# Kernel tuning notes

Measured on AMD Instinct MI355X. Metric: run time of the kernel, lower is better.

Reference implementation:

```python
import jax, jax.numpy as jnp
import numpy as np

N = 20000; E = 320000; G = 64; C_IN = 128; H = 128; L = 3; S = 4
EPS = 1e-5; SLOPE = 0.01  # GraphNorm eps, leaky_relu negative slope


def _kruskal(ei, ew, n):
    # Kruskal MST over edges sorted by usage-count weight; returns bidirectional MST edges
    # and the updated usage counts (used edges get +1), mirroring kruskal_mst_track_usage.
    order = np.argsort(ew, kind='stable')
    s = ei[0][order]; d = ei[1][order]
    parent = np.arange(n)
    def find(u):
        while parent[u] != u:
            parent[u] = parent[parent[u]]
            u = parent[u]
        return u
    mst = []; used = []
    for i in range(s.shape[0]):
        ru = find(s[i]); rv = find(d[i])
        if ru != rv:
            parent[ru] = rv
            mst.append((s[i], d[i]))
            used.append(order[i])
            if len(mst) == n - 1:
                break
    ew = ew.copy(); ew[np.asarray(used)] += 1
    m = np.asarray(mst, dtype=np.int64).T  # [2, ~n-1]
    return np.concatenate([m, m[::-1]], axis=1), ew  # bidirectional


def setup_inputs():
    rng = np.random.default_rng(0)
    x = rng.standard_normal((N, C_IN), dtype=np.float32)
    edge_index = rng.integers(0, N, size=(2, E)).astype(np.int64)
    batch = np.sort(rng.integers(0, G, size=N)).astype(np.int64)
    # split_graph: shuffle edges, then repeatedly extract MSTs (no_grad / CPU in original)
    perm = rng.permutation(E)
    ei_p = edge_index[:, perm]
    ew = np.zeros(E, dtype=np.int64)
    msts = []
    for _ in range(S - 1):  # only splits 0..3 are used; split 0 is the shuffled full graph
        m, ew = _kruskal(ei_p, ew, N)
        msts.append(m)
    def gp(shape):
        return jnp.asarray((0.05 * rng.standard_normal(shape)).astype(np.float32))
    return {
        'x': jnp.asarray(x),
        'emb_W': gp((C_IN, H)), 'emb_b': gp((H,)),
        'main_W': gp((L, H, H)), 'main_b': gp((L, H)),
        'main_gw': jnp.ones((L, H), jnp.float32), 'main_gb': jnp.zeros((L, H), jnp.float32), 'main_gms': jnp.ones((L, H), jnp.float32),
        'loc_W': gp((L, H, H)), 'loc_b': gp((L, H)),
        'loc_gw': jnp.ones((L, H), jnp.float32), 'loc_gb': jnp.zeros((L, H), jnp.float32), 'loc_gms': jnp.ones((L, H), jnp.float32),
        'merge_W': gp((H * (S + 1), H)), 'merge_b': gp((H,)),
        'edge_index': jnp.asarray(edge_index),
        'edges0': jnp.asarray(ei_p),
        'edges1': jnp.asarray(msts[0]),
        'edges2': jnp.asarray(msts[1]),
        'edges3': jnp.asarray(msts[2]),
        'batch': jnp.asarray(batch),
    }


def _seg(v, idx, n):
    return jax.ops.segment_sum(v, idx, num_segments=n)


def _gcn(x, W, b, src, dst):
    # PyG GCNConv with self-loops and symmetric normalization
    n = x.shape[0]
    h = x @ W
    deg = _seg(jnp.ones(src.shape[0], x.dtype), dst, n) + 1.0
    dinv = jax.lax.rsqrt(deg)
    coef = (dinv[src] * dinv[dst])[:, None]
    out = _seg(h[src] * coef, dst, n) + h * (dinv * dinv)[:, None]  # neighbors + self-loop
    return out + b


def _graph_norm(x, batch, cnt, w, b, ms):
    # PyG GraphNorm: per-graph mean with learnable mean_scale, per-graph variance
    mean = _seg(x, batch, G) / cnt
    out = x - ms * mean[batch]
    var = _seg(out * out, batch, G) / cnt
    inv = jax.lax.rsqrt(var + EPS)
    return w * out * inv[batch] + b


def _gnn(x, src, dst, Ws, bs, gw, gb, gms, batch, cnt):
    hist = []
    for l in range(L):
        x = _gcn(x, Ws[l], bs[l], src, dst)
        x = _graph_norm(x, batch, cnt, gw[l], gb[l], gms[l])
        x = jax.nn.leaky_relu(x, SLOPE)
        hist.append(x)  # dropout in eval mode = identity
    return hist


def _forward(x, emb_W, emb_b, main_W, main_b, main_gw, main_gb, main_gms,
             loc_W, loc_b, loc_gw, loc_gb, loc_gms, merge_W, merge_b,
             edge_index, edges0, edges1, edges2, edges3, batch):
    cnt = jnp.maximum(_seg(jnp.ones(N, x.dtype), batch, G), 1.0)[:, None]  # [G,1]
    h = x @ emb_W + emb_b
    main_hist = _gnn(h, edge_index[0], edge_index[1], main_W, main_b, main_gw, main_gb, main_gms, batch, cnt)
    split_hists = [_gnn(h, e[0], e[1], loc_W, loc_b, loc_gw, loc_gb, loc_gms, batch, cnt)
                   for e in (edges0, edges1, edges2, edges3)]
    gs = []
    for l in range(L):
        xl = jnp.concatenate([sh[l] for sh in split_hists] + [main_hist[l]], axis=1)  # [N, 5H]
        xl = xl @ merge_W + merge_b
        gs.append(_seg(xl, batch, G) / cnt)  # global_mean_pool
    return jnp.mean(jnp.stack(gs), axis=0)  # [G, H]


def reference(x, emb_W, emb_b, main_W, main_b, main_gw, main_gb, main_gms,
              loc_W, loc_b, loc_gw, loc_gb, loc_gms, merge_W, merge_b,
              edge_index, edges0, edges1, edges2, edges3, batch):
    return _forward(x, emb_W, emb_b, main_W, main_b, main_gw, main_gb, main_gms,
                    loc_W, loc_b, loc_gw, loc_gb, loc_gms, merge_W, merge_b,
                    edge_index, edges0, edges1, edges2, edges3, batch)
```

## Files before the change

### kernel.cpp

```cpp
#include <hip/hip_runtime.h>

#define NN 20000
#define NNP 20032
#define NH 128
#define NG 64
#define NLAY 3
#define NCH 5
#define GEPS 1e-5f
#define GSLOPE 0.01f

typedef unsigned short u16;
typedef unsigned int u32;
typedef __attribute__((ext_vector_type(8))) short short8;
typedef __attribute__((ext_vector_type(4))) float float4v;
typedef __attribute__((ext_vector_type(2))) float f32x2;

__device__ __forceinline__ u16 f2bf(float f) {
  union { float f; u32 u; } v; v.f = f;
  u32 r = (v.u + 0x7fffu + ((v.u >> 16) & 1u)) >> 16;
  return (u16)r;
}

struct ZP {
  const u16* A[NCH];
  const u16* W[NCH];
  u16* Y[NCH];
  int ystride[NCH];
  u16* Xo[NCH];
  u16* Xn[NCH];
  const float* bias[NCH];
  const float* gw[NCH];
  const float* gb[NCH];
  const float* gms[NCH];
  int colbase[NCH];
};

struct ES4 {
  const int* e[4];
  int cnt[4];
  int off[4];
};


__global__ __launch_bounds__(1024) void k_scan(const int* __restrict__ deg,
                                               int* __restrict__ indptr,
                                               int* __restrict__ cursor,
                                               float* __restrict__ dinv,
                                               const int* __restrict__ batch,
                                               int* __restrict__ counts,
                                               int* __restrict__ gstart) {
  int s = blockIdx.x;
  int t = threadIdx.x;
  if (s == 4) {
    int g = t;
    if (g < NG) {
      auto lb = [&](int key) {
        int lo = 0, hi = NN;
        while (lo < hi) {
          int mid = (lo + hi) >> 1;
          if (batch[mid] < key) lo = mid + 1; else hi = mid;
        }
        return lo;
      };
      int a = lb(g), b = lb(g + 1);
      gstart[g] = a;
      counts[g] = b - a;
    }
    return;
  }
  const int* d = deg + s * NN;
  int* ip = indptr + s * (NN + 1);
  int* cu = cursor + s * (NN + 1);
  int lane = t & 63, wv = t >> 6;
  __shared__ int wsum[16];
  int run = 0;
  const int NT = (NN + 1023) / 1024;
  for (int tile = 0; tile < NT; tile++) {
    int idx = tile * 1024 + t;
    int v = 0;
    if (idx < NN) {
      v = d[idx];
      dinv[s * NN + idx] = rsqrtf((float)v + 1.0f);
    }
    int x = v;
#pragma unroll
    for (int o = 1; o < 64; o <<= 1) {
      int y = __shfl_up(x, o);
      if (lane >= o) x += y;
    }
    if (lane == 63) wsum[wv] = x;
    __syncthreads();
    if (wv == 0) {
      int y = (lane < 16) ? wsum[lane] : 0;
#pragma unroll
      for (int o = 1; o < 16; o <<= 1) {
        int z = __shfl_up(y, o);
        if (lane >= o) y += z;
      }
      if (lane < 16) wsum[lane] = y;
    }
    __syncthreads();
    int waveoff = (wv == 0) ? 0 : wsum[wv - 1];
    int excl = run + waveoff + x - v;
    if (idx < NN) { ip[idx] = excl; cu[idx] = excl; }
    run += wsum[15];
    __syncthreads();
  }
  if (t == 0) { ip[NN] = run; cu[NN] = run; }
}

__global__ void k_fill(ES4 es, const float* __restrict__ dinv, int* __restrict__ cursor,
                       u32* __restrict__ ent) {
  int s = blockIdx.y;
  int i = blockIdx.x * 256 + threadIdx.x;
  int E = es.cnt[s];
  if (i >= E) return;
  int src = es.e[s][i];
  int dst = es.e[s][E + i];
  int pos = atomicAdd(&cursor[s * (NN + 1) + dst], 1);
  float c = dinv[s * NN + src] * dinv[s * NN + dst];
  ent[es.off[s] + pos] = (u32)src | ((u32)f2bf(c) << 16);
}

__global__ __launch_bounds__(256) void k_setup(ES4 es, int* __restrict__ deg,
                                               const float* __restrict__ embW,
                                               const float* __restrict__ locW,
                                               const float* __restrict__ mainW,
                                               u16* __restrict__ wt) {
  int ybk = blockIdx.y;
  if (ybk < 4) {
    int s = ybk;
    int i = blockIdx.x * 256 + threadIdx.x;
    int E = es.cnt[s];
    if (i < E) atomicAdd(&deg[s * NN + es.e[s][E + i]], 1);
    return;
  }
  if (blockIdx.x >= 16) return;
  int mat = ybk - 4;
  const float* W = (mat == 0) ? embW : ((mat <= 3) ? locW + (mat - 1) * NH * NH
                                                   : mainW + (mat - 4) * NH * NH);
  int tile = blockIdx.x;
  int tk = (tile >> 2) * 32;
  int tn = (tile & 3) * 32;
  __shared__ float tl[32][33];
  int c = threadIdx.x & 31, r = threadIdx.x >> 5;
#pragma unroll
  for (int rr = 0; rr < 32; rr += 8)
    tl[r + rr][c] = W[(size_t)(tk + r + rr) * NH + tn + c];
  __syncthreads();
#pragma unroll
  for (int rr = 0; rr < 32; rr += 8)
    wt[(size_t)mat * NH * NH + (size_t)(tn + r + rr) * NH + tk + c] = f2bf(tl[c][r + rr]);
}


__global__ __launch_bounds__(256) void k_gemm0(const float* __restrict__ x,
                                               const u16* __restrict__ wt,
                                               const float* __restrict__ embb,
                                               u16* __restrict__ ydual) {
  __shared__ u16 As[64][136];
  __shared__ u16 Bs[128][136];
  int t = threadIdx.x;
  int row0 = blockIdx.x * 64;
  int c = t & 15, rs = t >> 4;
#pragma unroll
  for (int pass = 0; pass < 4; pass++) {
    int r = pass * 16 + rs;
    int gr = row0 + r;
    uint4 o = make_uint4(0, 0, 0, 0);
    if (gr < NN) {
      float4 a = *(const float4*)(x + (size_t)gr * NH + c * 8);
      float4 b = *(const float4*)(x + (size_t)gr * NH + c * 8 + 4);
      o.x = f2bf(a.x) | ((u32)f2bf(a.y) << 16);
      o.y = f2bf(a.z) | ((u32)f2bf(a.w) << 16);
      o.z = f2bf(b.x) | ((u32)f2bf(b.y) << 16);
      o.w = f2bf(b.z) | ((u32)f2bf(b.w) << 16);
    }
    *(uint4*)(&As[r][c * 8]) = o;
  }
#pragma unroll
  for (int pass = 0; pass < 8; pass++) {
    int n = pass * 16 + rs;
    *(uint4*)(&Bs[n][c * 8]) = *(const uint4*)(wt + (size_t)n * NH + c * 8);
  }
  __syncthreads();
  int lane = t & 63, w = t >> 6;
  int m16 = lane & 15, quad = lane >> 4;
  float4v acc[8];
#pragma unroll
  for (int i = 0; i < 8; i++) acc[i] = (float4v)(0.f);
#pragma unroll
  for (int kk = 0; kk < 4; kk++) {
    short8 av = *(const short8*)(&As[w * 16 + m16][kk * 32 + quad * 8]);
#pragma unroll
    for (int ct = 0; ct < 8; ct++) {
      short8 bv = *(const short8*)(&Bs[ct * 16 + m16][kk * 32 + quad * 8]);
      acc[ct] = __builtin_amdgcn_mfma_f32_16x16x32_bf16(av, bv, acc[ct], 0, 0, 0);
    }
  }
  __syncthreads();
#pragma unroll
  for (int ct = 0; ct < 8; ct++) {
    float bv = embb[ct * 16 + m16];
#pragma unroll
    for (int r = 0; r < 4; r++)
      As[w * 16 + quad * 4 + r][ct * 16 + m16] = f2bf(acc[ct][r] + bv);
  }
  {
    const u16* wl = wt + (size_t)1 * NH * NH;
#pragma unroll
    for (int pass = 0; pass < 8; pass++) {
      int n = pass * 16 + rs;
      *(uint4*)(&Bs[n][c * 8]) = *(const uint4*)(wl + (size_t)n * NH + c * 8);
    }
  }
  __syncthreads();
  float4v acc0[8];
#pragma unroll
  for (int i = 0; i < 8; i++) acc0[i] = (float4v)(0.f);
#pragma unroll
  for (int kk = 0; kk < 4; kk++) {
    short8 av = *(const short8*)(&As[w * 16 + m16][kk * 32 + quad * 8]);
#pragma unroll
    for (int ct = 0; ct < 8; ct++) {
      short8 bv = *(const short8*)(&Bs[ct * 16 + m16][kk * 32 + quad * 8]);
      acc0[ct] = __builtin_amdgcn_mfma_f32_16x16x32_bf16(av, bv, acc0[ct], 0, 0, 0);
    }
  }
  __syncthreads();
  {
    const u16* wm = wt + (size_t)4 * NH * NH;
#pragma unroll
    for (int pass = 0; pass < 8; pass++) {
      int n = pass * 16 + rs;
      *(uint4*)(&Bs[n][c * 8]) = *(const uint4*)(wm + (size_t)n * NH + c * 8);
    }
  }
  __syncthreads();
  float4v acc4[8];
#pragma unroll
  for (int i = 0; i < 8; i++) acc4[i] = (float4v)(0.f);
#pragma unroll
  for (int kk = 0; kk < 4; kk++) {
    short8 av = *(const short8*)(&As[w * 16 + m16][kk * 32 + quad * 8]);
#pragma unroll
    for (int ct = 0; ct < 8; ct++) {
      short8 bv = *(const short8*)(&Bs[ct * 16 + m16][kk * 32 + quad * 8]);
      acc4[ct] = __builtin_amdgcn_mfma_f32_16x16x32_bf16(av, bv, acc4[ct], 0, 0, 0);
    }
  }
  __syncthreads();
#pragma unroll
  for (int ct = 0; ct < 8; ct++) {
#pragma unroll
    for (int r = 0; r < 4; r++) {
      As[w * 16 + quad * 4 + r][ct * 16 + m16] = f2bf(acc0[ct][r]);
      Bs[w * 16 + quad * 4 + r][ct * 16 + m16] = f2bf(acc4[ct][r]);
    }
  }
  __syncthreads();
#pragma unroll
  for (int pass = 0; pass < 4; pass++) {
    int r = pass * 16 + rs;
    int gr = row0 + r;
    if (gr < NN) {
      *(uint4*)(ydual + (size_t)gr * 256 + c * 8) = *(const uint4*)(&As[r][c * 8]);
      *(uint4*)(ydual + (size_t)gr * 256 + 128 + c * 8) = *(const uint4*)(&Bs[r][c * 8]);
    }
  }
}

__global__ __launch_bounds__(256) void k_gemm_bf(ZP p) {
  int zi = blockIdx.y;
  const u16* __restrict__ A = p.A[zi];
  const u16* __restrict__ Wt = p.W[zi];
  u16* __restrict__ Y = p.Y[zi];
  int yst = p.ystride[zi];
  __shared__ u16 As[64][136];
  __shared__ u16 Bs[128][136];
  int t = threadIdx.x;
  int row0 = blockIdx.x * 64;
  int c = t & 15, rs = t >> 4;
#pragma unroll
  for (int pass = 0; pass < 4; pass++) {
    int r = pass * 16 + rs;
    *(uint4*)(&As[r][c * 8]) = *(const uint4*)(A + (size_t)(row0 + r) * NH + c * 8);
  }
#pragma unroll
  for (int pass = 0; pass < 8; pass++) {
    int n = pass * 16 + rs;
    *(uint4*)(&Bs[n][c * 8]) = *(const uint4*)(Wt + (size_t)n * NH + c * 8);
  }
  __syncthreads();
  int lane = t & 63, w = t >> 6;
  int m16 = lane & 15, quad = lane >> 4;
  float4v acc[8];
#pragma unroll
  for (int i = 0; i < 8; i++) acc[i] = (float4v)(0.f);
#pragma unroll
  for (int kk = 0; kk < 4; kk++) {
    short8 av = *(const short8*)(&As[w * 16 + m16][kk * 32 + quad * 8]);
#pragma unroll
    for (int ct = 0; ct < 8; ct++) {
      short8 bv = *(const short8*)(&Bs[ct * 16 + m16][kk * 32 + quad * 8]);
      acc[ct] = __builtin_amdgcn_mfma_f32_16x16x32_bf16(av, bv, acc[ct], 0, 0, 0);
    }
  }
  __syncthreads();
#pragma unroll
  for (int ct = 0; ct < 8; ct++) {
#pragma unroll
    for (int r = 0; r < 4; r++) {
      As[w * 16 + quad * 4 + r][ct * 16 + m16] = f2bf(acc[ct][r]);
    }
  }
  __syncthreads();
#pragma unroll
  for (int pass = 0; pass < 4; pass++) {
    int r = pass * 16 + rs;
    int gr = row0 + r;
    if (gr < NN) *(uint4*)(Y + (size_t)gr * yst + c * 8) = *(const uint4*)(&As[r][c * 8]);
  }
}

__device__ __forceinline__ f32x2 bf2x2(u32 v) {
  f32x2 r;
  r.x = __uint_as_float(v << 16);
  r.y = __uint_as_float(v & 0xffff0000u);
  return r;
}

__device__ __forceinline__ void fma8p(f32x2* a, uint4 v, float cf) {
  f32x2 c2; c2.x = cf; c2.y = cf;
  a[0] += c2 * bf2x2(v.x);
  a[1] += c2 * bf2x2(v.y);
  a[2] += c2 * bf2x2(v.z);
  a[3] += c2 * bf2x2(v.w);
}

__device__ __forceinline__ void fin_chain(const float* a, const u16* Yb, int st, int node,
                                          int fo, float d2, const float* bias,
                                          u16* __restrict__ Xo) {
  uint4 sv = *(const uint4*)(Yb + (size_t)node * st + fo);
  float s[8] = {
    __uint_as_float(sv.x << 16), __uint_as_float(sv.x & 0xffff0000u),
    __uint_as_float(sv.y << 16), __uint_as_float(sv.y & 0xffff0000u),
    __uint_as_float(sv.z << 16), __uint_as_float(sv.z & 0xffff0000u),
    __uint_as_float(sv.w << 16), __uint_as_float(sv.w & 0xffff0000u)};
  float4 b0 = *(const float4*)(bias + fo);
  float4 b1 = *(const float4*)(bias + fo + 4);
  float bb[8] = {b0.x, b0.y, b0.z, b0.w, b1.x, b1.y, b1.z, b1.w};
  float o[8];
#pragma unroll
  for (int j = 0; j < 8; j++) o[j] = a[j] + d2 * s[j] + bb[j];
  uint4 ou;
  u32* op = (u32*)&ou;
#pragma unroll
  for (int j = 0; j < 4; j++)
    op[j] = (u32)f2bf(o[2 * j]) | ((u32)f2bf(o[2 * j + 1]) << 16);
  *(uint4*)(Xo + (size_t)node * NH + fo) = ou;
}

__global__ __launch_bounds__(256) void k_agg2(ZP p, const int* __restrict__ indptr,
                                              const u32* __restrict__ ent,
                                              const float* __restrict__ dinv, int4 entoff) {
  int b = blockIdx.x;
  int wv = threadIdx.x >> 6, lane = threadIdx.x & 63;
  int g = lane >> 4;
  int fo = (lane & 15) * 8;
  if (b < 5000) {
    int node = b * 4 + wv;
    int beg = indptr[node], end = indptr[node + 1];
    const u16* __restrict__ Y0 = p.Y[0];
    const u16* __restrict__ Y4 = p.Y[4];
    int st = p.ystride[0];
    f32x2 a0[4], a4[4];
#pragma unroll
    for (int j = 0; j < 4; j++) { a0[j] = (f32x2)(0.f); a4[j] = (f32x2)(0.f); }
    int e = beg + g;
    for (; e + 4 < end; e += 8) {
      u32 sa = ent[e];
      u32 sb = ent[e + 4];
      size_t ra = (size_t)(sa & 0xffffu) * st + fo;
      size_t rb = (size_t)(sb & 0xffffu) * st + fo;
      uint4 va0 = *(const uint4*)(Y0 + ra);
      uint4 va4 = *(const uint4*)(Y4 + ra);
      uint4 vb0 = *(const uint4*)(Y0 + rb);
      uint4 vb4 = *(const uint4*)(Y4 + rb);
      float ca = __uint_as_float(sa & 0xffff0000u);
      float cb = __uint_as_float(sb & 0xffff0000u);
      fma8p(a0, va0, ca); fma8p(a4, va4, ca);
      fma8p(a0, vb0, cb); fma8p(a4, vb4, cb);
    }
    if (e < end) {
      u32 sc = ent[e];
      float cf = __uint_as_float(sc & 0xffff0000u);
      size_t ro = (size_t)(sc & 0xffffu) * st + fo;
      uint4 v0 = *(const uint4*)(Y0 + ro);
      uint4 v4 = *(const uint4*)(Y4 + ro);
      fma8p(a0, v0, cf);
      fma8p(a4, v4, cf);
    }
    float* f0 = (float*)a0;
    float* f4 = (float*)a4;
#pragma unroll
    for (int j = 0; j < 8; j++) {
      f0[j] += __shfl_xor(f0[j], 16);
      f0[j] += __shfl_xor(f0[j], 32);
      f4[j] += __shfl_xor(f4[j], 16);
      f4[j] += __shfl_xor(f4[j], 32);
    }
    if (g == 0) {
      float di = dinv[node];
      float d2 = di * di;
      fin_chain(f0, Y0, st, node, fo, d2, p.bias[0], p.Xo[0]);
      fin_chain(f4, Y4, st, node, fo, d2, p.bias[4], p.Xo[4]);
    }
  } else {
    int mb = b - 5000;
    int s = 1 + mb / 1250;
    int node = (mb % 1250) * 16 + wv * 4 + g;
    const int* ip = indptr + s * (NN + 1);
    int eb = (s == 1) ? entoff.y : ((s == 2) ? entoff.z : entoff.w);
    const u16* __restrict__ Y = p.Y[s];
    int st = p.ystride[s];
    int beg = ip[node], end = ip[node + 1];
    const u32* __restrict__ ev = ent + eb;
    f32x2 a[4];
#pragma unroll
    for (int j = 0; j < 4; j++) a[j] = (f32x2)(0.f);
    for (int e = beg; e < end; e++) {
      u32 sc = ev[e];
      uint4 v = *(const uint4*)(Y + (size_t)(sc & 0xffffu) * st + fo);
      fma8p(a, v, __uint_as_float(sc & 0xffff0000u));
    }
    float di = dinv[s * NN + node];
    float d2 = di * di;
    fin_chain((float*)a, Y, st, node, fo, d2, p.bias[s], p.Xo[s]);
  }
}

__global__ __launch_bounds__(256) void k_norm2(ZP p, const int* __restrict__ gstart,
                                               const int* __restrict__ counts,
                                               float* __restrict__ Ml) {
  int g = blockIdx.x, zi = blockIdx.y, fc = blockIdx.z;
  const u16* __restrict__ X = p.Xo[zi];
  u16* __restrict__ Xn = p.Xn[zi];
  int t = threadIdx.x;
  int fj = t & 15;
  int f2 = fc * 32 + fj * 2;
  int rh = t >> 4;
  int start = gstart[g], cnt = counts[g];
  __shared__ float red[4][16][17];
  float s0 = 0.f, s1 = 0.f, q0 = 0.f, q1 = 0.f;
  for (int i = rh; i < cnt; i += 16) {
    u32 v = *(const u32*)(X + (size_t)(start + i) * NH + f2);
    float v0 = __uint_as_float(v << 16), v1 = __uint_as_float(v & 0xffff0000u);
    s0 += v0; q0 += v0 * v0;
    s1 += v1; q1 += v1 * v1;
  }
  red[0][rh][fj] = s0; red[1][rh][fj] = s1;
  red[2][rh][fj] = q0; red[3][rh][fj] = q1;
  __syncthreads();
#pragma unroll
  for (int off = 8; off >= 1; off >>= 1) {
    if (rh < off) {
      red[0][rh][fj] += red[0][rh + off][fj];
      red[1][rh][fj] += red[1][rh + off][fj];
      red[2][rh][fj] += red[2][rh + off][fj];
      red[3][rh][fj] += red[3][rh + off][fj];
    }
    __syncthreads();
  }
  float cntf = fmaxf((float)cnt, 1.f);
  float w0 = p.gw[zi][f2], w1 = p.gw[zi][f2 + 1];
  float b0 = p.gb[zi][f2], b1 = p.gb[zi][f2 + 1];
  float ms0 = p.gms[zi][f2], ms1 = p.gms[zi][f2 + 1];
  float mean0 = red[0][0][fj] / cntf, mean1 = red[1][0][fj] / cntf;
  float var0 = red[2][0][fj] / cntf - (2.f * ms0 - ms0 * ms0) * mean0 * mean0;
  float var1 = red[3][0][fj] / cntf - (2.f * ms1 - ms1 * ms1) * mean1 * mean1;
  float inv0 = rsqrtf(var0 + GEPS), inv1 = rsqrtf(var1 + GEPS);
  __syncthreads();
  float m0 = 0.f, m1 = 0.f;
  for (int i = rh; i < cnt; i += 16) {
    size_t ro = (size_t)(start + i) * NH + f2;
    u32 v = *(const u32*)(X + ro);
    float v0 = __uint_as_float(v << 16), v1 = __uint_as_float(v & 0xffff0000u);
    float o0 = w0 * (v0 - ms0 * mean0) * inv0 + b0;
    float o1 = w1 * (v1 - ms1 * mean1) * inv1 + b1;
    o0 = (o0 >= 0.f) ? o0 : GSLOPE * o0;
    o1 = (o1 >= 0.f) ? o1 : GSLOPE * o1;
    if (Xn) *(u32*)(Xn + ro) = (u32)f2bf(o0) | ((u32)f2bf(o1) << 16);
    m0 += o0; m1 += o1;
  }
  red[0][rh][fj] = m0; red[1][rh][fj] = m1;
  __syncthreads();
#pragma unroll
  for (int off = 8; off >= 1; off >>= 1) {
    if (rh < off) {
      red[0][rh][fj] += red[0][rh + off][fj];
      red[1][rh][fj] += red[1][rh + off][fj];
    }
    __syncthreads();
  }
  if (rh == 0) {
    int col = p.colbase[zi] + f2;
    Ml[(size_t)g * 640 + col] = red[0][0][fj];
    Ml[(size_t)g * 640 + col + 1] = red[1][0][fj];
  }
}

__global__ __launch_bounds__(256) void k_mergeout(const float* __restrict__ M,
                                                  const float* __restrict__ mergeW,
                                                  const float* __restrict__ mergeb,
                                                  const int* __restrict__ counts,
                                                  float* __restrict__ out) {
  int g = blockIdx.x;
  int f = threadIdx.x & 127, h = threadIdx.x >> 7;
  __shared__ float mrow[640];
  __shared__ float red[128];
  float acc = 0.f;
  for (int l = 0; l < NLAY; l++) {
    const float* Mr = M + ((size_t)l * NG + g) * 640;
    for (int i = threadIdx.x; i < 640; i += 256) mrow[i] = Mr[i];
    __syncthreads();
    float s = 0.f;
    int k0 = h * 320;
#pragma unroll 8
    for (int k = k0; k < k0 + 320; k++) s += mrow[k] * mergeW[(size_t)k * NH + f];
    if (h) red[f] = s;
    __syncthreads();
    if (!h) acc += s + red[f];
    __syncthreads();
  }
  if (!h) {
    float cnt = fmaxf((float)counts[g], 1.f);
    out[(size_t)g * NH + f] = acc / (3.f * cnt) + mergeb[f];
  }
}


struct Offs {
  size_t counts, gstart, deg, M, dinv, indptr, cursor, ent, wt, ydual;
  size_t yb[NCH], xo[NCH], xn[NCH];
  size_t memset1_off, memset1_len, total;
};

static size_t build_offs(Offs& o, int Etot) {
  size_t off = 0;
  auto alloc = [&](size_t bytes) -> size_t {
    off = (off + 255) & ~(size_t)255;
    size_t s = off;
    off += bytes;
    return s;
  };
  o.counts = alloc(NG * 4);
  o.gstart = alloc(NG * 4);
  o.deg = alloc((size_t)4 * NN * 4);
  o.memset1_off = o.deg;
  o.memset1_len = (size_t)4 * NN * 4;
  o.M = alloc((size_t)NLAY * NG * 640 * 4);
  o.dinv = alloc((size_t)4 * NN * 4);
  o.indptr = alloc((size_t)4 * (NN + 1) * 4);
  o.cursor = alloc((size_t)4 * (NN + 1) * 4);
  o.ent = alloc((size_t)Etot * 4);
  o.wt = alloc((size_t)7 * NH * NH * 2);
  o.ydual = alloc((size_t)NN * 256 * 2);
  for (int i = 1; i < 4; i++) o.yb[i] = alloc((size_t)NN * NH * 2);
  for (int i = 0; i < NCH; i++) {
    o.xo[i] = alloc((size_t)NN * NH * 2);
    o.xn[i] = alloc((size_t)NNP * NH * 2);
  }
  o.total = off;
  return off;
}

extern "C" void kernel_launch(void* const* d_in, const int* in_sizes, int n_in,
                              void* d_out, int out_size, void* d_ws, size_t ws_size,
                              hipStream_t stream) {
  if (n_in < 21) return;
  const float* x = (const float*)d_in[0];
  const float* embW = (const float*)d_in[1];
  const float* embb = (const float*)d_in[2];
  const float* mainW = (const float*)d_in[3];
  const float* mainb = (const float*)d_in[4];
  const float* maingw = (const float*)d_in[5];
  const float* maingb = (const float*)d_in[6];
  const float* maingms = (const float*)d_in[7];
  const float* locW = (const float*)d_in[8];
  const float* locb = (const float*)d_in[9];
  const float* locgw = (const float*)d_in[10];
  const float* locgb = (const float*)d_in[11];
  const float* locgms = (const float*)d_in[12];
  const float* mergeW = (const float*)d_in[13];
  const float* mergeb = (const float*)d_in[14];
  const int* edge_index = (const int*)d_in[15];
  const int* edges1 = (const int*)d_in[17];
  const int* edges2 = (const int*)d_in[18];
  const int* edges3 = (const int*)d_in[19];
  const int* batch = (const int*)d_in[20];

  int E0 = in_sizes[15] / 2;
  int E1 = in_sizes[17] / 2, E2 = in_sizes[18] / 2, E3 = in_sizes[19] / 2;
  int Etot = E0 + E1 + E2 + E3;
  int maxE = E0 > E1 ? E0 : E1;
  maxE = maxE > E2 ? maxE : E2;
  maxE = maxE > E3 ? maxE : E3;

  Offs o;
  if (build_offs(o, Etot) > ws_size) return;

  char* ws = (char*)d_ws;
  int* counts = (int*)(ws + o.counts);
  int* gstart = (int*)(ws + o.gstart);
  int* deg = (int*)(ws + o.deg);
  float* M = (float*)(ws + o.M);
  float* dinv = (float*)(ws + o.dinv);
  int* indptr = (int*)(ws + o.indptr);
  int* cursor = (int*)(ws + o.cursor);
  u32* ent = (u32*)(ws + o.ent);
  u16* wt = (u16*)(ws + o.wt);
  u16* ydual = (u16*)(ws + o.ydual);
  u16 *yb[NCH], *xo[NCH], *xn[NCH];
  for (int i = 1; i < 4; i++) yb[i] = (u16*)(ws + o.yb[i]);
  for (int i = 0; i < NCH; i++) {
    xo[i] = (u16*)(ws + o.xo[i]);
    xn[i] = (u16*)(ws + o.xn[i]);
  }

  ES4 es;
  es.e[0] = edge_index; es.e[1] = edges1; es.e[2] = edges2; es.e[3] = edges3;
  es.cnt[0] = E0; es.cnt[1] = E1; es.cnt[2] = E2; es.cnt[3] = E3;
  es.off[0] = 0; es.off[1] = E0; es.off[2] = E0 + E1; es.off[3] = E0 + E1 + E2;
  int4 entoff = make_int4(0, E0, E0 + E1, E0 + E1 + E2);

  hipMemsetAsync(ws + o.memset1_off, 0, o.memset1_len, stream);
  k_setup<<<dim3((maxE + 255) / 256, 11), 256, 0, stream>>>(es, deg, embW, locW, mainW, wt);
  k_scan<<<5, 1024, 0, stream>>>(deg, indptr, cursor, dinv, batch, counts, gstart);
  k_fill<<<dim3((maxE + 255) / 256, 4), 256, 0, stream>>>(es, dinv, cursor, ent);

  const int nrb = (NN + 63) / 64;

  k_gemm0<<<nrb, 256, 0, stream>>>(x, wt, embb, ydual);

  for (int l = 0; l < NLAY; l++) {
    ZP p = {};
    for (int zi = 0; zi < NCH; zi++) {
      bool isMain = (zi == 4);
      p.A[zi] = (const u16*)xn[zi];
      p.W[zi] = wt + (size_t)((isMain ? 4 : 1) + l) * NH * NH;
      if (zi == 0) { p.Y[0] = ydual; p.ystride[0] = 256; }
      else if (zi == 4) { p.Y[4] = ydual + 128; p.ystride[4] = 256; }
      else { p.Y[zi] = yb[zi]; p.ystride[zi] = 128; }
      p.Xo[zi] = xo[zi];
      p.Xn[zi] = (l == NLAY - 1) ? (u16*)nullptr : xn[zi];
      p.bias[zi] = (isMain ? mainb : locb) + (size_t)l * NH;
      p.gw[zi] = (isMain ? maingw : locgw) + (size_t)l * NH;
      p.gb[zi] = (isMain ? maingb : locgb) + (size_t)l * NH;
      p.gms[zi] = (isMain ? maingms : locgms) + (size_t)l * NH;
      p.colbase[zi] = isMain ? 512 : zi * NH;
    }
    if (l == 0) {
      p.Y[1] = ydual; p.Y[2] = ydual; p.Y[3] = ydual;
      p.ystride[1] = p.ystride[2] = p.ystride[3] = 256;
    } else {
      k_gemm_bf<<<dim3(nrb, NCH), 256, 0, stream>>>(p);
    }
    k_agg2<<<8750, 256, 0, stream>>>(p, indptr, ent, dinv, entoff);
    k_norm2<<<dim3(NG, NCH, 4), 256, 0, stream>>>(p, gstart, counts,
                                                  M + (size_t)l * NG * 640);
  }

  k_mergeout<<<NG, 256, 0, stream>>>(M, mergeW, mergeb, counts, (float*)d_out);
}
```

Measured before the change: 381.9 us.

## Fuse GraphNorm apply and leaky-relu into next layer's GEMM load

k_norm2 no longer writes the normalized activations. It stores per-graph mean*ms and inverse-std vectors, and k_gemm_bf applies the affine normalization plus leaky_relu while loading its A tile, using batch to look up each row's graph. This removes one full write and re-read of the [N,128] bf16 tensor per branch per layer, at the cost of a per-row batch lookup and extra per-graph stats loads inside the GEMM. The edge aggregation loop for the split graphs is also unrolled by two so two gathers are in flight at once.

```diff
diff --git a/kernel.cpp b/kernel.cpp
--- a/kernel.cpp
+++ b/kernel.cpp
@@ -27,11 +27,12 @@
   u16* Y[NCH];
   int ystride[NCH];
   u16* Xo[NCH];
-  u16* Xn[NCH];
   const float* bias[NCH];
   const float* gw[NCH];
   const float* gb[NCH];
   const float* gms[NCH];
+  const float* pgw[NCH];
+  const float* pgb[NCH];
   int colbase[NCH];
 };
 
@@ -270,21 +271,54 @@
   }
 }
 
-__global__ __launch_bounds__(256) void k_gemm_bf(ZP p) {
+__global__ __launch_bounds__(256) void k_gemm_bf(ZP p, const int* __restrict__ batch,
+                                                 const float* __restrict__ aff) {
   int zi = blockIdx.y;
-  const u16* __restrict__ A = p.A[zi];
+  const u16* __restrict__ X = p.A[zi];
   const u16* __restrict__ Wt = p.W[zi];
   u16* __restrict__ Y = p.Y[zi];
+  const float* __restrict__ gw = p.pgw[zi];
+  const float* __restrict__ gb = p.pgb[zi];
   int yst = p.ystride[zi];
   __shared__ u16 As[64][136];
   __shared__ u16 Bs[128][136];
   int t = threadIdx.x;
   int row0 = blockIdx.x * 64;
   int c = t & 15, rs = t >> 4;
+  float4 wA = *(const float4*)(gw + c * 8);
+  float4 wB = *(const float4*)(gw + c * 8 + 4);
+  float4 bA = *(const float4*)(gb + c * 8);
+  float4 bB = *(const float4*)(gb + c * 8 + 4);
+  float wv8[8] = {wA.x, wA.y, wA.z, wA.w, wB.x, wB.y, wB.z, wB.w};
+  float bv8[8] = {bA.x, bA.y, bA.z, bA.w, bB.x, bB.y, bB.z, bB.w};
 #pragma unroll
   for (int pass = 0; pass < 4; pass++) {
     int r = pass * 16 + rs;
-    *(uint4*)(&As[r][c * 8]) = *(const uint4*)(A + (size_t)(row0 + r) * NH + c * 8);
+    int gr = row0 + r;
+    int grc = (gr < NN) ? gr : (NN - 1);
+    int gg = batch[grc];
+    const float* ab = aff + ((size_t)zi * NG + gg) * 2 * NH;
+    uint4 xv = *(const uint4*)(X + (size_t)grc * NH + c * 8);
+    float4 mA = *(const float4*)(ab + c * 8);
+    float4 mB = *(const float4*)(ab + c * 8 + 4);
+    float4 iA = *(const float4*)(ab + NH + c * 8);
+    float4 iB = *(const float4*)(ab + NH + c * 8 + 4);
+    float mm[8] = {mA.x, mA.y, mA.z, mA.w, mB.x, mB.y, mB.z, mB.w};
+    float iv[8] = {iA.x, iA.y, iA.z, iA.w, iB.x, iB.y, iB.z, iB.w};
+    u32 xw[4] = {xv.x, xv.y, xv.z, xv.w};
+    uint4 ou;
+    u32* op = (u32*)&ou;
+#pragma unroll
+    for (int j = 0; j < 4; j++) {
+      float v0 = __uint_as_float(xw[j] << 16);
+      float v1 = __uint_as_float(xw[j] & 0xffff0000u);
+      float o0 = wv8[2 * j] * (v0 - mm[2 * j]) * iv[2 * j] + bv8[2 * j];
+      float o1 = wv8[2 * j + 1] * (v1 - mm[2 * j + 1]) * iv[2 * j + 1] + bv8[2 * j + 1];
+      o0 = (o0 >= 0.f) ? o0 : GSLOPE * o0;
+      o1 = (o1 >= 0.f) ? o1 : GSLOPE * o1;
+      op[j] = (u32)f2bf(o0) | ((u32)f2bf(o1) << 16);
+    }
+    *(uint4*)(&As[r][c * 8]) = ou;
   }
 #pragma unroll
   for (int pass = 0; pass < 8; pass++) {
@@ -429,7 +463,16 @@
     f32x2 a[4];
 #pragma unroll
     for (int j = 0; j < 4; j++) a[j] = (f32x2)(0.f);
-    for (int e = beg; e < end; e++) {
+    int e = beg;
+    for (; e + 1 < end; e += 2) {
+      u32 s0 = ev[e];
+      u32 s1 = ev[e + 1];
+      uint4 v0 = *(const uint4*)(Y + (size_t)(s0 & 0xffffu) * st + fo);
+      uint4 v1 = *(const uint4*)(Y + (size_t)(s1 & 0xffffu) * st + fo);
+      fma8p(a, v0, __uint_as_float(s0 & 0xffff0000u));
+      fma8p(a, v1, __uint_as_float(s1 & 0xffff0000u));
+    }
+    if (e < end) {
       u32 sc = ev[e];
       uint4 v = *(const uint4*)(Y + (size_t)(sc & 0xffffu) * st + fo);
       fma8p(a, v, __uint_as_float(sc & 0xffff0000u));
@@ -442,10 +485,10 @@
 
 __global__ __launch_bounds__(256) void k_norm2(ZP p, const int* __restrict__ gstart,
                                                const int* __restrict__ counts,
-                                               float* __restrict__ Ml) {
+                                               float* __restrict__ Ml,
+                                               float* __restrict__ aff) {
   int g = blockIdx.x, zi = blockIdx.y, fc = blockIdx.z;
   const u16* __restrict__ X = p.Xo[zi];
-  u16* __restrict__ Xn = p.Xn[zi];
   int t = threadIdx.x;
   int fj = t & 15;
   int f2 = fc * 32 + fj * 2;
@@ -477,6 +520,7 @@
   float b0 = p.gb[zi][f2], b1 = p.gb[zi][f2 + 1];
   float ms0 = p.gms[zi][f2], ms1 = p.gms[zi][f2 + 1];
   float mean0 = red[0][0][fj] / cntf, mean1 = red[1][0][fj] / cntf;
+  float mm0 = ms0 * mean0, mm1 = ms1 * mean1;
   float var0 = red[2][0][fj] / cntf - (2.f * ms0 - ms0 * ms0) * mean0 * mean0;
   float var1 = red[3][0][fj] / cntf - (2.f * ms1 - ms1 * ms1) * mean1 * mean1;
   float inv0 = rsqrtf(var0 + GEPS), inv1 = rsqrtf(var1 + GEPS);
@@ -486,11 +530,10 @@
     size_t ro = (size_t)(start + i) * NH + f2;
     u32 v = *(const u32*)(X + ro);
     float v0 = __uint_as_float(v << 16), v1 = __uint_as_float(v & 0xffff0000u);
-    float o0 = w0 * (v0 - ms0 * mean0) * inv0 + b0;
-    float o1 = w1 * (v1 - ms1 * mean1) * inv1 + b1;
+    float o0 = w0 * (v0 - mm0) * inv0 + b0;
+    float o1 = w1 * (v1 - mm1) * inv1 + b1;
     o0 = (o0 >= 0.f) ? o0 : GSLOPE * o0;
     o1 = (o1 >= 0.f) ? o1 : GSLOPE * o1;
-    if (Xn) *(u32*)(Xn + ro) = (u32)f2bf(o0) | ((u32)f2bf(o1) << 16);
     m0 += o0; m1 += o1;
   }
   red[0][rh][fj] = m0; red[1][rh][fj] = m1;
@@ -507,6 +550,11 @@
     int col = p.colbase[zi] + f2;
     Ml[(size_t)g * 640 + col] = red[0][0][fj];
     Ml[(size_t)g * 640 + col + 1] = red[1][0][fj];
+    if (aff) {
+      float* ab = aff + ((size_t)zi * NG + g) * 2 * NH;
+      ab[f2] = mm0; ab[f2 + 1] = mm1;
+      ab[NH + f2] = inv0; ab[NH + f2 + 1] = inv1;
+    }
   }
 }
 
@@ -541,8 +589,8 @@
 
 
 struct Offs {
-  size_t counts, gstart, deg, M, dinv, indptr, cursor, ent, wt, ydual;
-  size_t yb[NCH], xo[NCH], xn[NCH];
+  size_t counts, gstart, deg, M, dinv, indptr, cursor, ent, wt, ydual, aff;
+  size_t yb[NCH], xo[NCH];
   size_t memset1_off, memset1_len, total;
 };
 
@@ -565,11 +613,11 @@
   o.cursor = alloc((size_t)4 * (NN + 1) * 4);
   o.ent = alloc((size_t)Etot * 4);
   o.wt = alloc((size_t)7 * NH * NH * 2);
+  o.aff = alloc((size_t)NCH * NG * 2 * NH * 4);
   o.ydual = alloc((size_t)NN * 256 * 2);
   for (int i = 1; i < 4; i++) o.yb[i] = alloc((size_t)NN * NH * 2);
   for (int i = 0; i < NCH; i++) {
-    o.xo[i] = alloc((size_t)NN * NH * 2);
-    o.xn[i] = alloc((size_t)NNP * NH * 2);
+    o.xo[i] = alloc((size_t)NNP * NH * 2);
   }
   o.total = off;
   return off;
@@ -620,13 +668,11 @@
   int* cursor = (int*)(ws + o.cursor);
   u32* ent = (u32*)(ws + o.ent);
   u16* wt = (u16*)(ws + o.wt);
+  float* aff = (float*)(ws + o.aff);
   u16* ydual = (u16*)(ws + o.ydual);
-  u16 *yb[NCH], *xo[NCH], *xn[NCH];
+  u16 *yb[NCH], *xo[NCH];
   for (int i = 1; i < 4; i++) yb[i] = (u16*)(ws + o.yb[i]);
-  for (int i = 0; i < NCH; i++) {
-    xo[i] = (u16*)(ws + o.xo[i]);
-    xn[i] = (u16*)(ws + o.xn[i]);
-  }
+  for (int i = 0; i < NCH; i++) xo[i] = (u16*)(ws + o.xo[i]);
 
   ES4 es;
   es.e[0] = edge_index; es.e[1] = edges1; es.e[2] = edges2; es.e[3] = edges3;
@@ -644,31 +690,34 @@
   k_gemm0<<<nrb, 256, 0, stream>>>(x, wt, embb, ydual);
 
   for (int l = 0; l < NLAY; l++) {
+    int lp = (l > 0) ? (l - 1) : 0;
     ZP p = {};
     for (int zi = 0; zi < NCH; zi++) {
       bool isMain = (zi == 4);
-      p.A[zi] = (const u16*)xn[zi];
+      p.A[zi] = (const u16*)xo[zi];
       p.W[zi] = wt + (size_t)((isMain ? 4 : 1) + l) * NH * NH;
       if (zi == 0) { p.Y[0] = ydual; p.ystride[0] = 256; }
       else if (zi == 4) { p.Y[4] = ydual + 128; p.ystride[4] = 256; }
       else { p.Y[zi] = yb[zi]; p.ystride[zi] = 128; }
       p.Xo[zi] = xo[zi];
-      p.Xn[zi] = (l == NLAY - 1) ? (u16*)nullptr : xn[zi];
       p.bias[zi] = (isMain ? mainb : locb) + (size_t)l * NH;
       p.gw[zi] = (isMain ? maingw : locgw) + (size_t)l * NH;
       p.gb[zi] = (isMain ? maingb : locgb) + (size_t)l * NH;
       p.gms[zi] = (isMain ? maingms : locgms) + (size_t)l * NH;
+      p.pgw[zi] = (isMain ? maingw : locgw) + (size_t)lp * NH;
+      p.pgb[zi] = (isMain ? maingb : locgb) + (size_t)lp * NH;
       p.colbase[zi] = isMain ? 512 : zi * NH;
     }
     if (l == 0) {
       p.Y[1] = ydual; p.Y[2] = ydual; p.Y[3] = ydual;
       p.ystride[1] = p.ystride[2] = p.ystride[3] = 256;
     } else {
-      k_gemm_bf<<<dim3(nrb, NCH), 256, 0, stream>>>(p);
+      k_gemm_bf<<<dim3(nrb, NCH), 256, 0, stream>>>(p, batch, aff);
     }
     k_agg2<<<8750, 256, 0, stream>>>(p, indptr, ent, dinv, entoff);
     k_norm2<<<dim3(NG, NCH, 4), 256, 0, stream>>>(p, gstart, counts,
-                                                  M + (size_t)l * NG * 640);
+                                                  M + (size_t)l * NG * 640,
+                                                  (l == NLAY - 1) ? nullptr : aff);
   }
 
   k_mergeout<<<NG, 256, 0, stream>>>(M, mergeW, mergeb, counts, (float*)d_out);
```

Measured after the change: 376.3 us. No clear change (-1.5%).
